# Optimization experiments

Measured on AMD Instinct MI355X. Metric: run time of the kernel, lower is better.

## Reference

```python
import jax, jax.numpy as jnp
import numpy as np

DIM = 64      # channels C
RES = 128     # input_resolution (H = W)
WIN = 16      # ka_win_num
KS = 3        # kernel_size
WS = RES // int(np.sqrt(WIN))   # window_size = 32
NW = RES // WS                  # 4 windows per side
B = 4


def _dw_conv(x, w, groups):
    # depthwise conv, stride 1, pad 1; x:(N,G,H,W), w:(G,1,k,k)
    return jax.lax.conv_general_dilated(
        x, w, window_strides=(1, 1), padding=((1, 1), (1, 1)),
        feature_group_count=groups,
        dimension_numbers=('NCHW', 'OIHW', 'NCHW'))


def setup_inputs() -> dict:
    key = jax.random.key(0)
    ks = jax.random.split(key, 12)
    f = lambda k, shape: jax.random.normal(k, shape, jnp.float32) * 0.02
    return dict(
        x=jax.random.normal(ks[0], (B, RES * RES, DIM), jnp.float32),
        # ConvLayer1 depthwise params: torch uses plain randn init
        conv1_w=jax.random.normal(ks[1], (WIN * DIM, 1, KS, KS), jnp.float32),
        dc_w=f(ks[2], (WIN, DIM)), dc_b=f(ks[3], (WIN,)),
        l1_w=f(ks[4], (4 * WIN, WIN)), l1_b=f(ks[5], (4 * WIN,)),
        l2_w=f(ks[6], (WIN, 4 * WIN)), l2_b=f(ks[7], (WIN,)),
        gk_w=f(ks[8], (WIN,)), gk_b=f(ks[9], ()),
        fus_w=f(ks[10], (DIM, (WIN + 1) * DIM)), fus_b=f(ks[11], (DIM,)),
    )


def reference(x, conv1_w, dc_w, dc_b, l1_w, l1_b, l2_w, l2_b,
              gk_w, gk_b, fus_w, fus_b):
    b = x.shape[0]
    # pad_feature_map is a no-op here (RES % WS == 0)
    xw = (x.reshape(b, NW, WS, NW, WS, DIM)
           .transpose(0, 1, 3, 5, 2, 4)
           .reshape(b, WIN * DIM, WS, WS))
    # convlayer1: depthwise 3x3 per (window, channel)
    win_conv = _dw_conv(xw, conv1_w, WIN * DIM)
    # WinKernel_Reweight: pool -> grouped 1x1 -> 1x1 -> GELU -> 1x1 -> sigmoid
    pooled = win_conv.mean(axis=(2, 3)).reshape(b, WIN, DIM)
    w = jnp.einsum('bwc,wc->bw', pooled, dc_w) + dc_b
    w = jax.nn.gelu(w @ l1_w.T + l1_b, approximate=False)   # torch GELU is exact
    w = jax.nn.sigmoid(w @ l2_w.T + l2_b)
    # reweight per-window depthwise kernels
    base = conv1_w.reshape(WIN, DIM, KS, KS)
    kernels = w[:, :, None, None, None] * base[None]
    # global kernel: 1x1 conv over window axis
    gk = jnp.einsum('w,bwdij->bdij', gk_w, kernels) + gk_b  # (B, DIM, KS, KS)
    all_k = jnp.concatenate([kernels, gk[:, None]], axis=1)
    all_k = all_k.reshape(b * (WIN + 1) * DIM, 1, KS, KS)
    # apply per-sample dynamic depthwise kernels on the full-res map
    xi = x.reshape(b, RES, RES, DIM).transpose(0, 3, 1, 2)  # (B, C, H, W)
    xr = jnp.tile(xi, (1, WIN + 1, 1, 1)).reshape(1, b * (WIN + 1) * DIM, RES, RES)
    y = _dw_conv(xr, all_k, b * (WIN + 1) * DIM)
    y = y.reshape(b, (WIN + 1) * DIM, RES, RES)
    # fusion 1x1 conv
    y = jnp.einsum('bchw,oc->bohw', y, fus_w) + fus_b[None, :, None, None]
    return y.transpose(0, 2, 3, 1).reshape(b, RES * RES, DIM)
```

## Files before the change

kernel.cpp:

```cpp
#include <hip/hip_runtime.h>
#include <math.h>

#define BB   4
#define DIM  64
#define RES  128
#define WIN  16
#define WS   32

typedef __attribute__((ext_vector_type(8))) short bf16x8;
typedef __attribute__((ext_vector_type(4))) float f32x4;

static __device__ __forceinline__ unsigned short bf16_rne(float f) {
  unsigned int u = __float_as_uint(f);
  u += 0x7FFFu + ((u >> 16) & 1u);
  return (unsigned short)(u >> 16);
}
static __device__ __forceinline__ float bf16_f(unsigned short h) {
  return __uint_as_float(((unsigned int)h) << 16);
}

__global__ __launch_bounds__(1024) void k_pooled(
    const float* __restrict__ x, const float* __restrict__ conv1_w,
    float* __restrict__ pooled)
{
  const int blk = blockIdx.x;
  const int b = blk >> 4, w = blk & 15;
  const int wy = w >> 2, wx = w & 3;
  const int c = threadIdx.x & 63, rg = threadIdx.x >> 6;
  const float* xb = x + (size_t)b * RES * RES * DIM + c;

  float T = 0.f, R0 = 0.f, RL = 0.f, C0 = 0.f, CL = 0.f;
  for (int ii = 0; ii < 2; ++ii) {
    const int i  = rg * 2 + ii;
    const int gr = wy * WS + i;
    const float* xr = xb + (size_t)(gr * RES + wx * WS) * DIM;
    float rs = 0.f, v0 = 0.f, vL = 0.f;
#pragma unroll 8
    for (int j = 0; j < 32; ++j) {
      float v = xr[(size_t)j * DIM];
      rs += v;
      if (j == 0)  v0 = v;
      if (j == 31) vL = v;
    }
    T += rs; C0 += v0; CL += vL;
    if (i == 0)  R0 += rs;
    if (i == 31) RL += rs;
  }

  __shared__ float part[16][5][64];
  part[rg][0][c] = T;  part[rg][1][c] = R0; part[rg][2][c] = RL;
  part[rg][3][c] = C0; part[rg][4][c] = CL;
  __syncthreads();

  if (threadIdx.x < 64) {
    const int cc = threadIdx.x;
    float t = 0, r0 = 0, rl = 0, c0 = 0, cl = 0;
#pragma unroll
    for (int q = 0; q < 16; ++q) {
      t += part[q][0][cc]; r0 += part[q][1][cc]; rl += part[q][2][cc];
      c0 += part[q][3][cc]; cl += part[q][4][cc];
    }
    const float* xc = x + (size_t)b * RES * RES * DIM + cc;
    const size_t b00 = (size_t)(wy * WS * RES + wx * WS) * DIM;
    const float x00 = xc[b00];
    const float x0L = xc[b00 + 31 * DIM];
    const float xL0 = xc[b00 + (size_t)31 * RES * DIM];
    const float xLL = xc[b00 + (size_t)31 * RES * DIM + 31 * DIM];

    const float* bw = conv1_w + (size_t)(w * DIM + cc) * 9;
    float p = 0.f;
#pragma unroll
    for (int ky = 0; ky < 3; ++ky) {
#pragma unroll
      for (int kx = 0; kx < 3; ++kx) {
        const int dy = ky - 1, dx = kx - 1;
        float S = t;
        if (dy == 1)  S -= r0;
        if (dy == -1) S -= rl;
        if (dx == 1)  S -= c0;
        if (dx == -1) S -= cl;
        if (dy == 1 && dx == 1)   S += x00;
        if (dy == 1 && dx == -1)  S += x0L;
        if (dy == -1 && dx == 1)  S += xL0;
        if (dy == -1 && dx == -1) S += xLL;
        p += bw[ky * 3 + kx] * S;
      }
    }
    pooled[blk * 64 + cc] = p * (1.0f / 1024.0f);
  }
}

__global__ __launch_bounds__(576) void k_keff(
    const float* __restrict__ pooled, const float* __restrict__ conv1_w,
    const float* __restrict__ dc_w, const float* __restrict__ dc_b,
    const float* __restrict__ l1_w, const float* __restrict__ l1_b,
    const float* __restrict__ l2_w, const float* __restrict__ l2_b,
    const float* __restrict__ gk_w, const float* __restrict__ gk_b,
    const float* __restrict__ fus_w,
    unsigned short* __restrict__ kT_hi, unsigned short* __restrict__ kT_lo)
{
  const int b = blockIdx.x >> 6, o = blockIdx.x & 63;
  const int tid = threadIdx.x;
  __shared__ float w1s[16], hs[64], w2s[16], gkws[16];

  if (tid < 16) {
    float s = dc_b[tid];
    const float* p  = pooled + b * 1024 + tid * 64;
    const float* dw = dc_w + tid * 64;
    for (int cc = 0; cc < 64; ++cc) s += p[cc] * dw[cc];
    w1s[tid] = s;
    gkws[tid] = gk_w[tid];
  }
  __syncthreads();
  if (tid < 64) {
    float s = l1_b[tid];
    for (int g = 0; g < 16; ++g) s += w1s[g] * l1_w[tid * 16 + g];
    hs[tid] = 0.5f * s * (1.0f + erff(s * 0.70710678118654752f));
  }
  __syncthreads();
  if (tid < 16) {
    float s = l2_b[tid];
    for (int j = 0; j < 64; ++j) s += hs[j] * l2_w[tid * 64 + j];
    w2s[tid] = 1.0f / (1.0f + expf(-s));
  }
  __syncthreads();

  const int tap = tid >> 6, c = tid & 63;
  const float f1 = fus_w[o * 1088 + 1024 + c];
  float acc = gk_b[0] * f1;
#pragma unroll
  for (int g = 0; g < 16; ++g) {
    acc += w2s[g] * conv1_w[(size_t)(g * 64 + c) * 9 + tap] *
           (fus_w[o * 1088 + g * 64 + c] + gkws[g] * f1);
  }
  const unsigned short h = bf16_rne(acc);
  const unsigned short lo = bf16_rne(acc - bf16_f(h));
  const size_t kidx = (size_t)(b * 64 + o) * 576 + tid;
  kT_hi[kidx] = h;
  kT_lo[kidx] = lo;
}

__global__ __launch_bounds__(256, 4) void k_conv(
    const float* __restrict__ x,
    const unsigned short* __restrict__ kT_hi,
    const unsigned short* __restrict__ kT_lo,
    const float* __restrict__ fus_b, float* __restrict__ out)
{
  const int bid = blockIdx.x;
  const int b = bid >> 8;
  const int rem = bid & 255;
  const int row = rem >> 1;
  const int colbase = (rem & 1) * 64;
  const int tid = threadIdx.x;
  const int l = tid & 63, wv = tid >> 6;
  const int l16 = l & 15, lq = l >> 4;

  __shared__ unsigned short xs_hi[3][68][40];
  __shared__ unsigned short xs_lo[3][68][40];

  f32x4 acc[4];
#pragma unroll
  for (int mf = 0; mf < 4; ++mf) acc[mf] = (f32x4){0.f, 0.f, 0.f, 0.f};

  const float* xb = x + (size_t)b * RES * RES * DIM;
  const unsigned short* khB = kT_hi + (size_t)b * 64 * 576;
  const unsigned short* klB = kT_lo + (size_t)b * 64 * 576;

  for (int ch = 0; ch < 2; ++ch) {
    const int c0 = ch * 32;
    for (int i = tid; i < 3 * 66 * 8; i += 256) {
      const int rr  = i / (66 * 8);
      const int rem2 = i - rr * (66 * 8);
      const int cs  = rem2 >> 3;
      const int c4  = rem2 & 7;
      const int col = colbase + cs - 1;
      const int grow = row - 1 + rr;
      float4 v = make_float4(0.f, 0.f, 0.f, 0.f);
      if (grow >= 0 && grow < RES && col >= 0 && col < RES)
        v = *(const float4*)(xb + (size_t)(grow * RES + col) * DIM + c0 + c4 * 4);
      const unsigned short h0 = bf16_rne(v.x), h1 = bf16_rne(v.y),
                           h2 = bf16_rne(v.z), h3 = bf16_rne(v.w);
      const unsigned short q0 = bf16_rne(v.x - bf16_f(h0)),
                           q1 = bf16_rne(v.y - bf16_f(h1)),
                           q2 = bf16_rne(v.z - bf16_f(h2)),
                           q3 = bf16_rne(v.w - bf16_f(h3));
      *(ushort4*)&xs_hi[rr][cs][c4 * 4] = make_ushort4(h0, h1, h2, h3);
      *(ushort4*)&xs_lo[rr][cs][c4 * 4] = make_ushort4(q0, q1, q2, q3);
    }
    __syncthreads();

#pragma unroll
    for (int tap = 0; tap < 9; ++tap) {
      const int dy = tap / 3 - 1, dx = tap % 3 - 1;
      const int kb = tap * 64 + c0 + lq * 8;
      const size_t ko = (size_t)(wv * 16 + l16) * 576 + kb;
      const bf16x8 Bh = *(const bf16x8*)(khB + ko);
      const bf16x8 Bl = *(const bf16x8*)(klB + ko);
#pragma unroll
      for (int mf = 0; mf < 4; ++mf) {
        const int cs = 1 + mf * 16 + l16 + dx;
        const bf16x8 Ah = *(const bf16x8*)&xs_hi[dy + 1][cs][lq * 8];
        const bf16x8 Al = *(const bf16x8*)&xs_lo[dy + 1][cs][lq * 8];
        acc[mf] = __builtin_amdgcn_mfma_f32_16x16x32_bf16(Ah, Bh, acc[mf], 0, 0, 0);
        acc[mf] = __builtin_amdgcn_mfma_f32_16x16x32_bf16(Ah, Bl, acc[mf], 0, 0, 0);
        acc[mf] = __builtin_amdgcn_mfma_f32_16x16x32_bf16(Al, Bh, acc[mf], 0, 0, 0);
      }
    }
    __syncthreads();
  }

  const float fb = fus_b[wv * 16 + l16];
  const size_t pbase = (size_t)b * RES * RES + (size_t)row * RES + colbase;
#pragma unroll
  for (int mf = 0; mf < 4; ++mf) {
    const int pc = mf * 16 + lq * 4;
#pragma unroll
    for (int r4 = 0; r4 < 4; ++r4) {
      out[(pbase + pc + r4) * DIM + wv * 16 + l16] = acc[mf][r4] + fb;
    }
  }
}

extern "C" void kernel_launch(void* const* d_in, const int* in_sizes, int n_in,
                              void* d_out, int out_size, void* d_ws, size_t ws_size,
                              hipStream_t stream) {
  const float* x       = (const float*)d_in[0];
  const float* conv1_w = (const float*)d_in[1];
  const float* dc_w    = (const float*)d_in[2];
  const float* dc_b    = (const float*)d_in[3];
  const float* l1_w    = (const float*)d_in[4];
  const float* l1_b    = (const float*)d_in[5];
  const float* l2_w    = (const float*)d_in[6];
  const float* l2_b    = (const float*)d_in[7];
  const float* gk_w    = (const float*)d_in[8];
  const float* gk_b    = (const float*)d_in[9];
  const float* fus_w   = (const float*)d_in[10];
  const float* fus_b   = (const float*)d_in[11];
  float* out = (float*)d_out;

  float* pooled = (float*)d_ws;
  unsigned short* kT_hi = (unsigned short*)((char*)d_ws + 16384);
  unsigned short* kT_lo = kT_hi + (size_t)BB * 64 * 576;

  hipLaunchKernelGGL(k_pooled, dim3(BB * WIN), dim3(1024), 0, stream,
                     x, conv1_w, pooled);
  hipLaunchKernelGGL(k_keff, dim3(BB * 64), dim3(576), 0, stream,
                     pooled, conv1_w, dc_w, dc_b, l1_w, l1_b, l2_w, l2_b,
                     gk_w, gk_b, fus_w, kT_hi, kT_lo);
  hipLaunchKernelGGL(k_conv, dim3(BB * RES * 2), dim3(256), 0, stream,
                     x, kT_hi, kT_lo, fus_b, out);
}
```

Before: 123.2 us.

## Split window pooling across more blocks and finish reduction in keff kernel

The pooling stage now launches four times as many blocks (256 instead of 64), each covering 8 rows of a window and writing partial sums to a workspace buffer. The final reduction of the partials and the 3x3 boundary correction move into k_keff, which every one of its 256 blocks repeats redundantly for its batch. The aim is to fill more compute units during the memory-bound pooling pass. The cost is extra global traffic for the partial sums and duplicated aggregation work in every k_keff block.

```diff
diff --git a/kernel.cpp b/kernel.cpp
--- a/kernel.cpp
+++ b/kernel.cpp
@@ -19,54 +19,80 @@
   return __uint_as_float(((unsigned int)h) << 16);
 }
 
-__global__ __launch_bounds__(1024) void k_pooled(
-    const float* __restrict__ x, const float* __restrict__ conv1_w,
-    float* __restrict__ pooled)
+__global__ __launch_bounds__(512) void k_pooled_a(
+    const float* __restrict__ x, float* __restrict__ part_g)
 {
   const int blk = blockIdx.x;
-  const int b = blk >> 4, w = blk & 15;
+  const int b = blk >> 6, w = (blk >> 2) & 15, st = blk & 3;
   const int wy = w >> 2, wx = w & 3;
   const int c = threadIdx.x & 63, rg = threadIdx.x >> 6;
-  const float* xb = x + (size_t)b * RES * RES * DIM + c;
-
-  float T = 0.f, R0 = 0.f, RL = 0.f, C0 = 0.f, CL = 0.f;
-  for (int ii = 0; ii < 2; ++ii) {
-    const int i  = rg * 2 + ii;
-    const int gr = wy * WS + i;
-    const float* xr = xb + (size_t)(gr * RES + wx * WS) * DIM;
-    float rs = 0.f, v0 = 0.f, vL = 0.f;
+  const int i = st * 8 + rg;
+  const int gr = wy * WS + i;
+  const float* xr = x + ((size_t)b * RES * RES + (size_t)gr * RES + wx * WS) * DIM + c;
+
+  float rs = 0.f, v0 = 0.f, vL = 0.f;
 #pragma unroll 8
-    for (int j = 0; j < 32; ++j) {
-      float v = xr[(size_t)j * DIM];
-      rs += v;
-      if (j == 0)  v0 = v;
-      if (j == 31) vL = v;
-    }
-    T += rs; C0 += v0; CL += vL;
-    if (i == 0)  R0 += rs;
-    if (i == 31) RL += rs;
-  }
-
-  __shared__ float part[16][5][64];
-  part[rg][0][c] = T;  part[rg][1][c] = R0; part[rg][2][c] = RL;
-  part[rg][3][c] = C0; part[rg][4][c] = CL;
-  __syncthreads();
-
-  if (threadIdx.x < 64) {
-    const int cc = threadIdx.x;
-    float t = 0, r0 = 0, rl = 0, c0 = 0, cl = 0;
-#pragma unroll
-    for (int q = 0; q < 16; ++q) {
-      t += part[q][0][cc]; r0 += part[q][1][cc]; rl += part[q][2][cc];
-      c0 += part[q][3][cc]; cl += part[q][4][cc];
-    }
-    const float* xc = x + (size_t)b * RES * RES * DIM + cc;
+  for (int j = 0; j < 32; ++j) {
+    float v = xr[(size_t)j * DIM];
+    rs += v;
+    if (j == 0)  v0 = v;
+    if (j == 31) vL = v;
+  }
+
+  __shared__ float part[8][5][64];
+  part[rg][0][c] = rs;
+  part[rg][1][c] = (i == 0)  ? rs : 0.f;
+  part[rg][2][c] = (i == 31) ? rs : 0.f;
+  part[rg][3][c] = v0;
+  part[rg][4][c] = vL;
+  __syncthreads();
+
+  if (threadIdx.x < 320) {
+    const int a = threadIdx.x >> 6, cc = threadIdx.x & 63;
+    float s = 0.f;
+#pragma unroll
+    for (int r = 0; r < 8; ++r) s += part[r][a][cc];
+    part_g[(((size_t)blk) * 5 + a) * 64 + cc] = s;
+  }
+}
+
+__global__ __launch_bounds__(576) void k_keff(
+    const float* __restrict__ x, const float* __restrict__ part_g,
+    const float* __restrict__ conv1_w,
+    const float* __restrict__ dc_w, const float* __restrict__ dc_b,
+    const float* __restrict__ l1_w, const float* __restrict__ l1_b,
+    const float* __restrict__ l2_w, const float* __restrict__ l2_b,
+    const float* __restrict__ gk_w, const float* __restrict__ gk_b,
+    const float* __restrict__ fus_w,
+    unsigned short* __restrict__ kT_hi, unsigned short* __restrict__ kT_lo)
+{
+  const int b = blockIdx.x >> 6, o = blockIdx.x & 63;
+  const int tid = threadIdx.x;
+  __shared__ float agg[5][16][64];
+  __shared__ float pooled_s[16][64];
+  __shared__ float w1s[16], hs[64], w2s[16], gkws[16];
+
+  for (int idx = tid; idx < 5 * 16 * 64; idx += 576) {
+    const int a = idx >> 10, rem = idx & 1023, w = rem >> 6, cc = rem & 63;
+    float s = 0.f;
+#pragma unroll
+    for (int st = 0; st < 4; ++st)
+      s += part_g[((((size_t)b * 16 + w) * 4 + st) * 5 + a) * 64 + cc];
+    agg[a][w][cc] = s;
+  }
+  __syncthreads();
+
+  for (int idx = tid; idx < 16 * 64; idx += 576) {
+    const int w = idx >> 6, cc = idx & 63;
+    const int wy = w >> 2, wx = w & 3;
+    const float* xb = x + (size_t)b * RES * RES * DIM + cc;
     const size_t b00 = (size_t)(wy * WS * RES + wx * WS) * DIM;
-    const float x00 = xc[b00];
-    const float x0L = xc[b00 + 31 * DIM];
-    const float xL0 = xc[b00 + (size_t)31 * RES * DIM];
-    const float xLL = xc[b00 + (size_t)31 * RES * DIM + 31 * DIM];
-
+    const float x00 = xb[b00];
+    const float x0L = xb[b00 + 31 * DIM];
+    const float xL0 = xb[b00 + (size_t)31 * RES * DIM];
+    const float xLL = xb[b00 + (size_t)31 * RES * DIM + 31 * DIM];
+    const float t  = agg[0][w][cc], r0 = agg[1][w][cc], rl = agg[2][w][cc],
+                c0 = agg[3][w][cc], cl = agg[4][w][cc];
     const float* bw = conv1_w + (size_t)(w * DIM + cc) * 9;
     float p = 0.f;
 #pragma unroll
@@ -86,28 +112,14 @@
         p += bw[ky * 3 + kx] * S;
       }
     }
-    pooled[blk * 64 + cc] = p * (1.0f / 1024.0f);
-  }
-}
-
-__global__ __launch_bounds__(576) void k_keff(
-    const float* __restrict__ pooled, const float* __restrict__ conv1_w,
-    const float* __restrict__ dc_w, const float* __restrict__ dc_b,
-    const float* __restrict__ l1_w, const float* __restrict__ l1_b,
-    const float* __restrict__ l2_w, const float* __restrict__ l2_b,
-    const float* __restrict__ gk_w, const float* __restrict__ gk_b,
-    const float* __restrict__ fus_w,
-    unsigned short* __restrict__ kT_hi, unsigned short* __restrict__ kT_lo)
-{
-  const int b = blockIdx.x >> 6, o = blockIdx.x & 63;
-  const int tid = threadIdx.x;
-  __shared__ float w1s[16], hs[64], w2s[16], gkws[16];
+    pooled_s[w][cc] = p * (1.0f / 1024.0f);
+  }
+  __syncthreads();
 
   if (tid < 16) {
     float s = dc_b[tid];
-    const float* p  = pooled + b * 1024 + tid * 64;
     const float* dw = dc_w + tid * 64;
-    for (int cc = 0; cc < 64; ++cc) s += p[cc] * dw[cc];
+    for (int cc = 0; cc < 64; ++cc) s += pooled_s[tid][cc] * dw[cc];
     w1s[tid] = s;
     gkws[tid] = gk_w[tid];
   }
@@ -238,14 +250,14 @@
   const float* fus_b   = (const float*)d_in[11];
   float* out = (float*)d_out;
 
-  float* pooled = (float*)d_ws;
-  unsigned short* kT_hi = (unsigned short*)((char*)d_ws + 16384);
+  float* part_g = (float*)d_ws;
+  unsigned short* kT_hi = (unsigned short*)((char*)d_ws + 327680);
   unsigned short* kT_lo = kT_hi + (size_t)BB * 64 * 576;
 
-  hipLaunchKernelGGL(k_pooled, dim3(BB * WIN), dim3(1024), 0, stream,
-                     x, conv1_w, pooled);
+  hipLaunchKernelGGL(k_pooled_a, dim3(BB * WIN * 4), dim3(512), 0, stream,
+                     x, part_g);
   hipLaunchKernelGGL(k_keff, dim3(BB * 64), dim3(576), 0, stream,
-                     pooled, conv1_w, dc_w, dc_b, l1_w, l1_b, l2_w, l2_b,
+                     x, part_g, conv1_w, dc_w, dc_b, l1_w, l1_b, l2_w, l2_b,
                      gk_w, gk_b, fus_w, kT_hi, kT_lo);
   hipLaunchKernelGGL(k_conv, dim3(BB * RES * 2), dim3(256), 0, stream,
                      x, kT_hi, kT_lo, fus_b, out);
```

Measured after the change: 124.5 us. About the same (+1.1%).
